# Optimization experiments

Measured on AMD Instinct MI355X. Metric: run time of the kernel, lower is better.

The kernel has to match this reference:

```python
import jax, jax.numpy as jnp
import numpy as np

# Coarse-to-fine lossless 3D segmentation (Seg3dLossless), batch=1, C=1.
RES = [17, 33, 65, 129]          # odd resolutions, stride (RF-1)/(R-1) is integral
RF = RES[-1]
B_MIN, B_MAX = -1.0, 1.0
BAL = 0.5                        # balance_value
N_CONFLICT_ITERS = 2             # fixed unroll of the data-dependent while-loop


def _mlp(pts, w1, b1, w2, b2, w3, b3):
    # query_func: occupancy MLP on normalized (x,y,z) points -> [N]
    h = jax.nn.relu(pts @ w1 + b1)
    h = jax.nn.relu(h @ w2 + b2)
    return jax.nn.sigmoid(h @ w3 + b3)[..., 0]


def _eval_grid(R, w1, b1, w2, b2, w3, b3):
    # batch_eval with align_corners=False: coords2D = (coord + 0.5)/RF, mapped to [B_MIN,B_MAX]
    s = (RF - 1) // (R - 1)
    c = jnp.arange(R, dtype=jnp.float32) * s                 # final-res integer coords
    p = (c + 0.5) / RF * (B_MAX - B_MIN) + B_MIN
    zz, yy, xx = jnp.meshgrid(p, p, p, indexing='ij')        # [D,H,W]
    pts = jnp.stack([xx, yy, zz], axis=-1).reshape(-1, 3)    # (x,y,z) order
    return _mlp(pts, w1, b1, w2, b2, w3, b3).reshape(R, R, R)


def _resize(x, R):
    # trilinear, align_corners=True: out index j -> in coord j*(in-1)/(out-1)
    c = jnp.linspace(0.0, x.shape[0] - 1.0, R)
    zz, yy, xx = jnp.meshgrid(c, c, c, indexing='ij')
    return jax.scipy.ndimage.map_coordinates(x, [zz, yy, xx], order=1, mode='nearest')


def _dilate(m):
    # smooth_conv3x3 (mean filter) followed by >0 == 3x3x3 binary dilation
    f = jax.lax.reduce_window(m.astype(jnp.float32), 0.0, jax.lax.max,
                              (3, 3, 3), (1, 1, 1), 'SAME')
    return f > 0.0


def setup_inputs() -> dict:
    key = jax.random.key(0)
    k1, k2, k3 = jax.random.split(key, 3)
    H = 64
    return {
        'w1': jax.random.normal(k1, (3, H), jnp.float32) * 0.8,
        'b1': jnp.zeros((H,), jnp.float32),
        'w2': jax.random.normal(k2, (H, H), jnp.float32) * (1.0 / np.sqrt(H)),
        'b2': jnp.zeros((H,), jnp.float32),
        'w3': jax.random.normal(k3, (H, 1), jnp.float32) * (1.0 / np.sqrt(H)),
        'b3': jnp.zeros((1,), jnp.float32),
    }


def reference(w1, b1, w2, b2, w3, b3):
    params = (w1, b1, w2, b2, w3, b3)
    # level 0: dense eval on the coarse grid
    occ = _eval_grid(RES[0], *params)                        # [R0,R0,R0]
    s0 = (RF - 1) // (RES[0] - 1)
    calculated = jnp.zeros((RF, RF, RF), bool).at[::s0, ::s0, ::s0].set(True)

    for R in RES[1:]:
        s = (RF - 1) // (R - 1)
        valid = _resize((occ > BAL).astype(jnp.float32), R)  # no-grad mask path
        occ_i = _resize(occ, R)                              # differentiable interp
        boundary = _dilate((valid > 0.0) & (valid < 1.0))
        calc_l = calculated[::s, ::s, ::s]
        boundary = boundary & (~calc_l)                      # skip already-evaluated voxels
        occ_true = _eval_grid(R, *params)                    # query_func at this level
        occ = jnp.where(boundary, occ_true, occ_i)           # scatter of occupancys_topk
        calc_l = calc_l | boundary
        # conflict resolution: re-query 3^3 neighbors of sign-flip voxels
        conflict = boundary & ((occ_i - BAL) * (occ_true - BAL) < 0.0)
        for _ in range(N_CONFLICT_ITERS):
            nbr = _dilate(conflict) & (~calc_l)
            occ_prev = occ
            occ = jnp.where(nbr, occ_true, occ)
            calc_l = calc_l | nbr
            conflict = nbr & ((occ_prev - BAL) * (occ_true - BAL) < 0.0)
        calculated = calculated.at[::s, ::s, ::s].set(calc_l)

    return occ[None, None]                                   # (1, 1, D, H, W)
```

## Files before the change

### kernel.cpp

```cpp
#include <hip/hip_runtime.h>

#define HH 64

static __global__ void k_set_ones(unsigned char* __restrict__ p, int n){
  int i = blockIdx.x * blockDim.x + threadIdx.x;
  if (i < n) p[i] = 1;
}

static __global__ void k_prep_w2t(const float* __restrict__ w2, float* __restrict__ w2t){
  int t = blockIdx.x * 256 + threadIdx.x;
  w2t[t] = w2[(t & 63) * HH + (t >> 6)];
}

__device__ __forceinline__ void mlp_pair(
    const float* __restrict__ sw1,
    const float* __restrict__ sw2t,
    const float* __restrict__ b2, const float* __restrict__ w3,
    const float* __restrict__ b3,
    float xA, float yA, float zA, float xB, float yB, float zB,
    float& outA, float& outB)
{
  const int ibase = ((threadIdx.x & 63) >> 5) * 32;
  float h1a[32], h1b[32];
  #pragma unroll
  for (int k = 0; k < 32; k += 4){
    const float4 wx = *(const float4*)&sw1[      ibase + k];
    const float4 wy = *(const float4*)&sw1[ 64 + ibase + k];
    const float4 wz = *(const float4*)&sw1[128 + ibase + k];
    const float4 bb = *(const float4*)&sw1[192 + ibase + k];
    h1a[k+0] = fmaxf(fmaf(xA,wx.x,fmaf(yA,wy.x,fmaf(zA,wz.x,bb.x))),0.f);
    h1a[k+1] = fmaxf(fmaf(xA,wx.y,fmaf(yA,wy.y,fmaf(zA,wz.y,bb.y))),0.f);
    h1a[k+2] = fmaxf(fmaf(xA,wx.z,fmaf(yA,wy.z,fmaf(zA,wz.z,bb.z))),0.f);
    h1a[k+3] = fmaxf(fmaf(xA,wx.w,fmaf(yA,wy.w,fmaf(zA,wz.w,bb.w))),0.f);
    h1b[k+0] = fmaxf(fmaf(xB,wx.x,fmaf(yB,wy.x,fmaf(zB,wz.x,bb.x))),0.f);
    h1b[k+1] = fmaxf(fmaf(xB,wx.y,fmaf(yB,wy.y,fmaf(zB,wz.y,bb.y))),0.f);
    h1b[k+2] = fmaxf(fmaf(xB,wx.z,fmaf(yB,wy.z,fmaf(zB,wz.z,bb.z))),0.f);
    h1b[k+3] = fmaxf(fmaf(xB,wx.w,fmaf(yB,wy.w,fmaf(zB,wz.w,bb.w))),0.f);
  }
  float oa = b3[0], ob = oa;
  #pragma unroll 1
  for (int j = 0; j < HH; ++j){
    const float4* wrow = (const float4*)&sw2t[j*HH + ibase];
    float a0 = 0.f, a1 = 0.f, c0 = 0.f, c1 = 0.f;
    #pragma unroll
    for (int q = 0; q < 8; q += 2){
      const float4 w0 = wrow[q];
      const float4 w1q = wrow[q+1];
      a0 = fmaf(h1a[4*q+0], w0.x, a0);
      a0 = fmaf(h1a[4*q+1], w0.y, a0);
      a0 = fmaf(h1a[4*q+2], w0.z, a0);
      a0 = fmaf(h1a[4*q+3], w0.w, a0);
      a1 = fmaf(h1a[4*q+4], w1q.x, a1);
      a1 = fmaf(h1a[4*q+5], w1q.y, a1);
      a1 = fmaf(h1a[4*q+6], w1q.z, a1);
      a1 = fmaf(h1a[4*q+7], w1q.w, a1);
      c0 = fmaf(h1b[4*q+0], w0.x, c0);
      c0 = fmaf(h1b[4*q+1], w0.y, c0);
      c0 = fmaf(h1b[4*q+2], w0.z, c0);
      c0 = fmaf(h1b[4*q+3], w0.w, c0);
      c1 = fmaf(h1b[4*q+4], w1q.x, c1);
      c1 = fmaf(h1b[4*q+5], w1q.y, c1);
      c1 = fmaf(h1b[4*q+6], w1q.z, c1);
      c1 = fmaf(h1b[4*q+7], w1q.w, c1);
    }
    float accA = a0 + a1, accB = c0 + c1;
    accA += __shfl_xor(accA, 32);
    accB += __shfl_xor(accB, 32);
    const float bj = b2[j], wj = w3[j];
    oa = fmaf(fmaxf(accA + bj, 0.f), wj, oa);
    ob = fmaf(fmaxf(accB + bj, 0.f), wj, ob);
  }
  outA = 1.f / (1.f + expf(-oa));
  outB = 1.f / (1.f + expf(-ob));
}

#define STAGE_WEIGHTS()                                            \
  __shared__ float sw1[4*HH];                                      \
  __shared__ float sw2t[HH*HH];                                    \
  {                                                                \
    const int t0 = threadIdx.x;                                    \
    if (t0 < 3*HH) sw1[t0] = w1[t0];                               \
    else sw1[t0] = b1[t0 - 3*HH];                                  \
    const float4* s4 = (const float4*)w2t;                         \
    float4* d4 = (float4*)sw2t;                                    \
    for (int i4 = t0; i4 < HH*HH/4; i4 += 256) d4[i4] = s4[i4];    \
    __syncthreads();                                               \
  }

static __global__ __launch_bounds__(256)
__attribute__((amdgpu_waves_per_eu(4,4)))
void k_eval_mlp(
    const float* __restrict__ w1, const float* __restrict__ b1,
    const float* __restrict__ w2t, const float* __restrict__ b2,
    const float* __restrict__ w3, const float* __restrict__ b3,
    float* __restrict__ out, int R, int s)
{
  STAGE_WEIGHTS();
  const unsigned int n = (unsigned int)R * (unsigned int)R * (unsigned int)R;
  const int lane = threadIdx.x & 63;
  const int wid = threadIdx.x >> 6;
  const unsigned int base = blockIdx.x * 256u + (unsigned int)(wid * 64 + (lane & 31));
  const unsigned int pidA = base < n ? base : (n - 1u);
  const unsigned int pB = base + 32u;
  const unsigned int pidB = pB < n ? pB : (n - 1u);
  const float inv129x2 = 2.0f / 129.0f;
  unsigned int cA = pidA % (unsigned int)R, rA = pidA / (unsigned int)R;
  unsigned int cB = pidB % (unsigned int)R, rB = pidB / (unsigned int)R;
  const float xA = ((float)(cA * (unsigned int)s) + 0.5f) * inv129x2 - 1.0f;
  const float yA = ((float)((rA % (unsigned int)R) * (unsigned int)s) + 0.5f) * inv129x2 - 1.0f;
  const float zA = ((float)((rA / (unsigned int)R) * (unsigned int)s) + 0.5f) * inv129x2 - 1.0f;
  const float xB = ((float)(cB * (unsigned int)s) + 0.5f) * inv129x2 - 1.0f;
  const float yB = ((float)((rB % (unsigned int)R) * (unsigned int)s) + 0.5f) * inv129x2 - 1.0f;
  const float zB = ((float)((rB / (unsigned int)R) * (unsigned int)s) + 0.5f) * inv129x2 - 1.0f;
  float oA, oB;
  mlp_pair(sw1, sw2t, b2, w3, b3, xA, yA, zA, xB, yB, zB, oA, oB);
  if ((threadIdx.x & 63) < 32){
    if (base < n) out[pidA] = oA;
    if (pB < n)   out[pidB] = oB;
  }
}

static __global__ __launch_bounds__(256)
__attribute__((amdgpu_waves_per_eu(4,4)))
void k_eval_sparse(
    const float* __restrict__ w1, const float* __restrict__ b1,
    const float* __restrict__ w2t, const float* __restrict__ b2,
    const float* __restrict__ w3, const float* __restrict__ b3,
    const int* __restrict__ idxl, const unsigned int* __restrict__ cnt,
    const float* __restrict__ occ_i,
    float* __restrict__ out, unsigned char* __restrict__ mism,
    int R, int s, unsigned int n)
{
  unsigned int count = *cnt;
  if (count > n) count = n;
  if (blockIdx.x * 256u >= count) return;
  STAGE_WEIGHTS();
  const int lane = threadIdx.x & 63;
  const int wid = threadIdx.x >> 6;
  const unsigned int slotA = blockIdx.x * 256u + (unsigned int)(wid * 64 + (lane & 31));
  const unsigned int slotB = slotA + 32u;
  const bool vA = slotA < count, vB = slotB < count;
  const unsigned int pidA = (unsigned int)idxl[vA ? slotA : 0];
  const unsigned int pidB = (unsigned int)idxl[vB ? slotB : 0];
  const float inv129x2 = 2.0f / 129.0f;
  unsigned int cA = pidA % (unsigned int)R, rA = pidA / (unsigned int)R;
  unsigned int cB = pidB % (unsigned int)R, rB = pidB / (unsigned int)R;
  const float xA = ((float)(cA * (unsigned int)s) + 0.5f) * inv129x2 - 1.0f;
  const float yA = ((float)((rA % (unsigned int)R) * (unsigned int)s) + 0.5f) * inv129x2 - 1.0f;
  const float zA = ((float)((rA / (unsigned int)R) * (unsigned int)s) + 0.5f) * inv129x2 - 1.0f;
  const float xB = ((float)(cB * (unsigned int)s) + 0.5f) * inv129x2 - 1.0f;
  const float yB = ((float)((rB % (unsigned int)R) * (unsigned int)s) + 0.5f) * inv129x2 - 1.0f;
  const float zB = ((float)((rB / (unsigned int)R) * (unsigned int)s) + 0.5f) * inv129x2 - 1.0f;
  float oA, oB;
  mlp_pair(sw1, sw2t, b2, w3, b3, xA, yA, zA, xB, yB, zB, oA, oB);
  if ((threadIdx.x & 63) < 32){
    if (vA){
      out[pidA] = oA;
      mism[pidA] = ((occ_i[pidA] - 0.5f) * (oA - 0.5f) < 0.0f) ? (unsigned char)1 : (unsigned char)0;
    }
    if (vB){
      out[pidB] = oB;
      mism[pidB] = ((occ_i[pidB] - 0.5f) * (oB - 0.5f) < 0.0f) ? (unsigned char)1 : (unsigned char)0;
    }
  }
}

static __global__ __launch_bounds__(256) void k_resize_b0(
    const float* __restrict__ prev,
    const unsigned char* __restrict__ calc_prev,
    float* __restrict__ occ_i, float* __restrict__ occ_out,
    unsigned char* __restrict__ bnd0, unsigned char* __restrict__ calc_out,
    unsigned char* __restrict__ confA, unsigned char* __restrict__ confB,
    unsigned char* __restrict__ upd, int R, int Rp)
{
  const unsigned int n = (unsigned int)R * (unsigned int)R * (unsigned int)R;
  unsigned int gid = blockIdx.x * 256u + threadIdx.x;
  if (gid >= n) return;
  int c = (int)(gid % (unsigned int)R);
  unsigned int r = gid / (unsigned int)R;
  int b = (int)(r % (unsigned int)R);
  int a = (int)(r / (unsigned int)R);
  int a0 = a >> 1, da = a & 1;
  int b0i = b >> 1, db = b & 1;
  int c0 = c >> 1, dc = c & 1;
  float sum = 0.0f;
  int cnt = 0;
  const int tot = (da + 1) * (db + 1) * (dc + 1);
  for (int dz = 0; dz <= da; ++dz)
    for (int dy = 0; dy <= db; ++dy)
      for (int dx = 0; dx <= dc; ++dx){
        float v = prev[((unsigned int)(a0 + dz) * (unsigned int)Rp + (unsigned int)(b0i + dy)) * (unsigned int)Rp + (unsigned int)(c0 + dx)];
        sum += v;
        cnt += (v > 0.5f) ? 1 : 0;
      }
  float oi = sum / (float)tot;
  occ_i[gid] = oi;
  occ_out[gid] = oi;
  bnd0[gid] = (cnt > 0 && cnt < tot) ? 1 : 0;
  calc_out[gid] = ((da | db | dc) == 0)
      ? calc_prev[((unsigned int)a0 * (unsigned int)Rp + (unsigned int)b0i) * (unsigned int)Rp + (unsigned int)c0]
      : (unsigned char)0;
  confA[gid] = 0; confB[gid] = 0; upd[gid] = 0;
}

static __global__ __launch_bounds__(256) void k_resize_boundary(
    const float* __restrict__ prev, const float* __restrict__ occ_true,
    const unsigned char* __restrict__ calc_prev,
    float* __restrict__ occ_i, float* __restrict__ occ_out,
    unsigned char* __restrict__ bnd0,
    unsigned char* __restrict__ mism, unsigned char* __restrict__ calc_out,
    int R, int Rp)
{
  const unsigned int n = (unsigned int)R * (unsigned int)R * (unsigned int)R;
  unsigned int gid = blockIdx.x * 256u + threadIdx.x;
  if (gid >= n) return;
  int c = (int)(gid % (unsigned int)R);
  unsigned int r = gid / (unsigned int)R;
  int b = (int)(r % (unsigned int)R);
  int a = (int)(r / (unsigned int)R);
  int a0 = a >> 1, da = a & 1;
  int b0i = b >> 1, db = b & 1;
  int c0 = c >> 1, dc = c & 1;
  float sum = 0.0f;
  int cnt = 0;
  const int tot = (da + 1) * (db + 1) * (dc + 1);
  for (int dz = 0; dz <= da; ++dz)
    for (int dy = 0; dy <= db; ++dy)
      for (int dx = 0; dx <= dc; ++dx){
        float v = prev[((unsigned int)(a0 + dz) * (unsigned int)Rp + (unsigned int)(b0i + dy)) * (unsigned int)Rp + (unsigned int)(c0 + dx)];
        sum += v;
        cnt += (v > 0.5f) ? 1 : 0;
      }
  float oi = sum / (float)tot;
  occ_i[gid] = oi;
  occ_out[gid] = oi;
  bnd0[gid] = (cnt > 0 && cnt < tot) ? 1 : 0;
  mism[gid] = ((oi - 0.5f) * (occ_true[gid] - 0.5f) < 0.0f) ? 1 : 0;
  calc_out[gid] = ((da | db | dc) == 0)
      ? calc_prev[((unsigned int)a0 * (unsigned int)Rp + (unsigned int)b0i) * (unsigned int)Rp + (unsigned int)c0]
      : (unsigned char)0;
}

static __global__ __launch_bounds__(256) void k_dil7x(
    const unsigned char* __restrict__ in, unsigned char* __restrict__ outp, int R)
{
  const unsigned int n = (unsigned int)R * (unsigned int)R * (unsigned int)R;
  unsigned int gid = blockIdx.x * 256u + threadIdx.x;
  if (gid >= n) return;
  int c = (int)(gid % (unsigned int)R);
  int g = (int)gid;
  int m = 0;
  #pragma unroll
  for (int d = -3; d <= 3; ++d){
    int q = c + d;
    if (q >= 0 && q < R) m |= in[g + d];
  }
  outp[gid] = (unsigned char)(m ? 1 : 0);
}

static __global__ __launch_bounds__(256) void k_dil7y(
    const unsigned char* __restrict__ in, unsigned char* __restrict__ outp, int R)
{
  const unsigned int n = (unsigned int)R * (unsigned int)R * (unsigned int)R;
  unsigned int gid = blockIdx.x * 256u + threadIdx.x;
  if (gid >= n) return;
  unsigned int r = gid / (unsigned int)R;
  int b = (int)(r % (unsigned int)R);
  int g = (int)gid;
  int m = 0;
  #pragma unroll
  for (int d = -3; d <= 3; ++d){
    int q = b + d;
    if (q >= 0 && q < R) m |= in[g + d * R];
  }
  outp[gid] = (unsigned char)(m ? 1 : 0);
}

static __global__ __launch_bounds__(256) void k_dil7z_count(
    const unsigned char* __restrict__ in, unsigned char* __restrict__ outp,
    unsigned int* __restrict__ bcnt, int R)
{
  const unsigned int n = (unsigned int)R * (unsigned int)R * (unsigned int)R;
  unsigned int gid = blockIdx.x * 256u + threadIdx.x;
  int m = 0;
  if (gid < n){
    int a = (int)(gid / ((unsigned int)R * (unsigned int)R));
    int g = (int)gid;
    int RR = R * R;
    #pragma unroll
    for (int d = -3; d <= 3; ++d){
      int q = a + d;
      if (q >= 0 && q < R) m |= in[g + d * RR];
    }
    outp[gid] = (unsigned char)(m ? 1 : 0);
  }
  unsigned long long bm = __ballot(m != 0);
  __shared__ unsigned int wc[4];
  int wid = (int)(threadIdx.x >> 6);
  if ((threadIdx.x & 63u) == 0) wc[wid] = (unsigned int)__popcll(bm);
  __syncthreads();
  if (threadIdx.x == 0) bcnt[blockIdx.x] = wc[0] + wc[1] + wc[2] + wc[3];
}

static __global__ __launch_bounds__(1024) void k_scan(
    unsigned int* __restrict__ bcnt, unsigned int nb, unsigned int* __restrict__ total)
{
  __shared__ unsigned int part[1024];
  const unsigned int t = threadIdx.x;
  const unsigned int chunk = (nb + 1023u) / 1024u;
  const unsigned int beg = t * chunk;
  const unsigned int end = (beg + chunk < nb) ? (beg + chunk) : nb;
  unsigned int s = 0;
  for (unsigned int i = beg; i < end; ++i) s += bcnt[i];
  part[t] = s;
  __syncthreads();
  for (int offd = 1; offd < 1024; offd <<= 1){
    unsigned int v = (t >= (unsigned int)offd) ? part[t - offd] : 0u;
    __syncthreads();
    part[t] += v;
    __syncthreads();
  }
  unsigned int run = (t == 0) ? 0u : part[t - 1];
  for (unsigned int i = beg; i < end; ++i){
    unsigned int v = bcnt[i];
    bcnt[i] = run;
    run += v;
  }
  if (t == 1023) *total = part[1023];
}

static __global__ __launch_bounds__(256) void k_scatter(
    const unsigned char* __restrict__ cand, const unsigned int* __restrict__ boff,
    int* __restrict__ idxl, unsigned int n)
{
  unsigned int gid = blockIdx.x * 256u + threadIdx.x;
  bool pred = (gid < n) && (cand[gid] != 0);
  unsigned long long m = __ballot(pred);
  __shared__ unsigned int wbase[4];
  int wid = (int)(threadIdx.x >> 6);
  int lane = (int)(threadIdx.x & 63u);
  if (lane == 0) wbase[wid] = (unsigned int)__popcll(m);
  __syncthreads();
  if (threadIdx.x == 0){
    unsigned int b = boff[blockIdx.x];
    unsigned int t0 = wbase[0], t1 = wbase[1], t2 = wbase[2];
    wbase[0] = b; wbase[1] = b + t0; wbase[2] = b + t0 + t1; wbase[3] = b + t0 + t1 + t2;
  }
  __syncthreads();
  if (pred){
    int pre = __popcll(m & ((1ull << lane) - 1ull));
    idxl[wbase[wid] + (unsigned int)pre] = (int)gid;
  }
}

static __global__ __launch_bounds__(256) void k_dilate_sparse(
    const int* __restrict__ idxl, const unsigned int* __restrict__ cnt,
    const unsigned char* __restrict__ src, const unsigned char* __restrict__ mism,
    unsigned char* __restrict__ calc, unsigned char* __restrict__ conf_out,
    unsigned char* __restrict__ upd, int R, int final_step,
    const float* __restrict__ occ_true, float* __restrict__ occ_out,
    unsigned int n)
{
  unsigned int count = *cnt;
  if (count > n) count = n;
  for (unsigned int slot = blockIdx.x * 256u + threadIdx.x; slot < count;
       slot += gridDim.x * 256u){
    int gid = idxl[slot];
    int c = gid % R;
    int r = gid / R;
    int b = r % R;
    int a = r / R;
    int m = 0;
    for (int dz = -1; dz <= 1; ++dz){
      int az = a + dz; if (az < 0 || az >= R) continue;
      for (int dy = -1; dy <= 1; ++dy){
        int by = b + dy; if (by < 0 || by >= R) continue;
        for (int dx = -1; dx <= 1; ++dx){
          int cx = c + dx; if (cx < 0 || cx >= R) continue;
          m |= src[(az * R + by) * R + cx];
        }
      }
    }
    unsigned char nb = (m && !calc[gid]) ? (unsigned char)1 : (unsigned char)0;
    conf_out[gid] = (nb && mism[gid]) ? (unsigned char)1 : (unsigned char)0;
    unsigned char u = upd[gid];
    if (nb){ calc[gid] = 1; if (!u){ upd[gid] = 1; u = 1; } }
    if (final_step && u) occ_out[gid] = occ_true[gid];
  }
}

static __global__ __launch_bounds__(256) void k_dilate_step(
    const unsigned char* __restrict__ src, const unsigned char* __restrict__ mism,
    unsigned char* __restrict__ calc, unsigned char* __restrict__ conf_out,
    unsigned char* __restrict__ upd, int R, int first, int final_step,
    const float* __restrict__ occ_true, float* __restrict__ occ_out)
{
  const unsigned int n = (unsigned int)R * (unsigned int)R * (unsigned int)R;
  unsigned int gid = blockIdx.x * 256u + threadIdx.x;
  if (gid >= n) return;
  int c = (int)(gid % (unsigned int)R);
  unsigned int r = gid / (unsigned int)R;
  int b = (int)(r % (unsigned int)R);
  int a = (int)(r / (unsigned int)R);
  int m = 0;
  for (int dz = -1; dz <= 1; ++dz){
    int az = a + dz; if (az < 0 || az >= R) continue;
    for (int dy = -1; dy <= 1; ++dy){
      int by = b + dy; if (by < 0 || by >= R) continue;
      for (int dx = -1; dx <= 1; ++dx){
        int cx = c + dx; if (cx < 0 || cx >= R) continue;
        m |= src[((unsigned int)az * (unsigned int)R + (unsigned int)by) * (unsigned int)R + (unsigned int)cx];
      }
    }
  }
  unsigned char nb = (m && !calc[gid]) ? (unsigned char)1 : (unsigned char)0;
  if (nb) calc[gid] = 1;
  conf_out[gid] = (nb && mism[gid]) ? (unsigned char)1 : (unsigned char)0;
  unsigned char u;
  if (first){ u = nb; upd[gid] = nb; }
  else { u = upd[gid]; if (nb && !u){ upd[gid] = 1; u = 1; } }
  if (final_step && u) occ_out[gid] = occ_true[gid];
}

extern "C" void kernel_launch(void* const* d_in, const int* in_sizes, int n_in,
                              void* d_out, int out_size, void* d_ws, size_t ws_size,
                              hipStream_t stream)
{
  const float* w1 = (const float*)d_in[0];
  const float* b1 = (const float*)d_in[1];
  const float* w2 = (const float*)d_in[2];
  const float* b2 = (const float*)d_in[3];
  const float* w3 = (const float*)d_in[4];
  const float* b3 = (const float*)d_in[5];
  float* out = (float*)d_out;

  const int NF = 129 * 129 * 129;
  const int NP = 65 * 65 * 65;
  char* ws = (char*)d_ws;
  size_t off = 0;
  auto alloc = [&](size_t bytes) -> void* {
    void* p = (void*)(ws + off);
    off += (bytes + 255) & ~(size_t)255;
    return p;
  };
  float* f_true  = (float*)alloc((size_t)NF * 4);
  float* f_occi  = (float*)alloc((size_t)NF * 4);
  float* f_prevA = (float*)alloc((size_t)NP * 4);
  float* f_prevB = (float*)alloc((size_t)NP * 4);
  float* f_w2t   = (float*)alloc((size_t)HH * HH * 4);
  int*   i_idx   = (int*)alloc((size_t)NF * 4);
  unsigned int* u_cnt  = (unsigned int*)alloc(256);
  unsigned int* u_bcnt = (unsigned int*)alloc(8448 * 4);
  unsigned char* b_b0    = (unsigned char*)alloc(NF);
  unsigned char* b_mism  = (unsigned char*)alloc(NF);
  unsigned char* b_confA = (unsigned char*)alloc(NF);
  unsigned char* b_confB = (unsigned char*)alloc(NF);
  unsigned char* b_calcA = (unsigned char*)alloc(NF);
  unsigned char* b_calcB = (unsigned char*)alloc(NF);
  unsigned char* b_upd   = (unsigned char*)alloc(NF);
  unsigned char* b_cand  = (unsigned char*)alloc(NF);
  unsigned char* b_tmp   = (unsigned char*)alloc(NF);
  (void)ws_size;

  k_prep_w2t<<<16, 256, 0, stream>>>(w2, f_w2t);

  {
    int R = 17, s = 8;
    int n = R * R * R;
    int blocks = (n + 255) / 256;
    k_eval_mlp<<<blocks, 256, 0, stream>>>(w1, b1, f_w2t, b2, w3, b3, f_prevA, R, s);
    k_set_ones<<<blocks, 256, 0, stream>>>(b_calcA, n);
  }

  int Rp = 17;
  float* prev = f_prevA;
  unsigned char* calcP = b_calcA;
  unsigned char* calcC = b_calcB;
  for (int li = 1; li <= 3; ++li){
    int R = 2 * Rp - 1;
    int s = 128 / (R - 1);
    unsigned int n = (unsigned int)R * (unsigned int)R * (unsigned int)R;
    int blocks = (int)((n + 255u) / 256u);
    float* occ_out = (li == 3) ? out : ((prev == f_prevA) ? f_prevB : f_prevA);

    if (R == 33){
      k_eval_mlp<<<blocks, 256, 0, stream>>>(w1, b1, f_w2t, b2, w3, b3, f_true, R, s);
      k_resize_boundary<<<blocks, 256, 0, stream>>>(prev, f_true, calcP, f_occi, occ_out, b_b0, b_mism, calcC, R, Rp);
      k_dilate_step<<<blocks, 256, 0, stream>>>(b_b0,    b_mism, calcC, b_confA, b_upd, R, 1, 0, f_true, occ_out);
      k_dilate_step<<<blocks, 256, 0, stream>>>(b_confA, b_mism, calcC, b_confB, b_upd, R, 0, 0, f_true, occ_out);
      k_dilate_step<<<blocks, 256, 0, stream>>>(b_confB, b_mism, calcC, b_confA, b_upd, R, 0, 1, f_true, occ_out);
    } else {
      k_resize_b0<<<blocks, 256, 0, stream>>>(prev, calcP, f_occi, occ_out, b_b0, calcC,
                                              b_confA, b_confB, b_upd, R, Rp);
      k_dil7x<<<blocks, 256, 0, stream>>>(b_b0,  b_tmp,  R);
      k_dil7y<<<blocks, 256, 0, stream>>>(b_tmp, b_cand, R);
      k_dil7z_count<<<blocks, 256, 0, stream>>>(b_cand, b_tmp, u_bcnt, R);
      k_scan<<<1, 1024, 0, stream>>>(u_bcnt, (unsigned int)blocks, u_cnt);
      k_scatter<<<blocks, 256, 0, stream>>>(b_tmp, u_bcnt, i_idx, n);
      k_eval_sparse<<<blocks, 256, 0, stream>>>(
          w1, b1, f_w2t, b2, w3, b3, i_idx, u_cnt, f_occi, f_true, b_mism, R, s, n);
      int sblocks = blocks < 4096 ? blocks : 4096;
      k_dilate_sparse<<<sblocks, 256, 0, stream>>>(i_idx, u_cnt, b_b0,    b_mism, calcC, b_confA, b_upd, R, 0, f_true, occ_out, n);
      k_dilate_sparse<<<sblocks, 256, 0, stream>>>(i_idx, u_cnt, b_confA, b_mism, calcC, b_confB, b_upd, R, 0, f_true, occ_out, n);
      k_dilate_sparse<<<sblocks, 256, 0, stream>>>(i_idx, u_cnt, b_confB, b_mism, calcC, b_confA, b_upd, R, 1, f_true, occ_out, n);
    }

    prev = occ_out;
    unsigned char* tmpc = calcP; calcP = calcC; calcC = tmpc;
    Rp = R;
  }
  (void)in_sizes; (void)n_in; (void)out_size;
}
```

Before: 307.4 us.

## Evaluate MLP one point per thread reading weights directly from global memory

Replaces the paired-point, split-hidden-dimension MLP (two points per thread, halves reduced with a cross-lane shuffle, weights staged in LDS) with a one-point-per-thread version. Each thread keeps all 64 hidden activations in registers and reads w1/w2t/b2/w3 straight from global memory through uniform loads, so the shared-memory staging and its __syncthreads are gone. This raises per-thread register pressure (64-float array under a 4-waves-per-EU bound) and depends on the weight loads being wave-uniform and cached, which could cause spills or slower weight fetches.

New measurement: 348.3 us. 13.3% more time.

```diff
diff --git a/kernel.cpp b/kernel.cpp
--- a/kernel.cpp
+++ b/kernel.cpp
@@ -12,80 +12,32 @@
   w2t[t] = w2[(t & 63) * HH + (t >> 6)];
 }
 
-__device__ __forceinline__ void mlp_pair(
-    const float* __restrict__ sw1,
-    const float* __restrict__ sw2t,
-    const float* __restrict__ b2, const float* __restrict__ w3,
-    const float* __restrict__ b3,
-    float xA, float yA, float zA, float xB, float yB, float zB,
-    float& outA, float& outB)
-{
-  const int ibase = ((threadIdx.x & 63) >> 5) * 32;
-  float h1a[32], h1b[32];
+__device__ __forceinline__ float mlp_point(
+    const float* __restrict__ w1, const float* __restrict__ b1,
+    const float* __restrict__ w2t, const float* __restrict__ b2,
+    const float* __restrict__ w3, const float* __restrict__ b3,
+    float x, float y, float z)
+{
+  float h[HH];
   #pragma unroll
-  for (int k = 0; k < 32; k += 4){
-    const float4 wx = *(const float4*)&sw1[      ibase + k];
-    const float4 wy = *(const float4*)&sw1[ 64 + ibase + k];
-    const float4 wz = *(const float4*)&sw1[128 + ibase + k];
-    const float4 bb = *(const float4*)&sw1[192 + ibase + k];
-    h1a[k+0] = fmaxf(fmaf(xA,wx.x,fmaf(yA,wy.x,fmaf(zA,wz.x,bb.x))),0.f);
-    h1a[k+1] = fmaxf(fmaf(xA,wx.y,fmaf(yA,wy.y,fmaf(zA,wz.y,bb.y))),0.f);
-    h1a[k+2] = fmaxf(fmaf(xA,wx.z,fmaf(yA,wy.z,fmaf(zA,wz.z,bb.z))),0.f);
-    h1a[k+3] = fmaxf(fmaf(xA,wx.w,fmaf(yA,wy.w,fmaf(zA,wz.w,bb.w))),0.f);
-    h1b[k+0] = fmaxf(fmaf(xB,wx.x,fmaf(yB,wy.x,fmaf(zB,wz.x,bb.x))),0.f);
-    h1b[k+1] = fmaxf(fmaf(xB,wx.y,fmaf(yB,wy.y,fmaf(zB,wz.y,bb.y))),0.f);
-    h1b[k+2] = fmaxf(fmaf(xB,wx.z,fmaf(yB,wy.z,fmaf(zB,wz.z,bb.z))),0.f);
-    h1b[k+3] = fmaxf(fmaf(xB,wx.w,fmaf(yB,wy.w,fmaf(zB,wz.w,bb.w))),0.f);
-  }
-  float oa = b3[0], ob = oa;
-  #pragma unroll 1
+  for (int k = 0; k < HH; ++k)
+    h[k] = fmaxf(fmaf(x, w1[k], fmaf(y, w1[HH + k], fmaf(z, w1[2*HH + k], b1[k]))), 0.f);
+  float o = b3[0];
+  #pragma unroll 2
   for (int j = 0; j < HH; ++j){
-    const float4* wrow = (const float4*)&sw2t[j*HH + ibase];
-    float a0 = 0.f, a1 = 0.f, c0 = 0.f, c1 = 0.f;
+    const float* __restrict__ row = w2t + j * HH;
+    float a0 = 0.f, a1 = 0.f, a2 = 0.f, a3 = 0.f;
     #pragma unroll
-    for (int q = 0; q < 8; q += 2){
-      const float4 w0 = wrow[q];
-      const float4 w1q = wrow[q+1];
-      a0 = fmaf(h1a[4*q+0], w0.x, a0);
-      a0 = fmaf(h1a[4*q+1], w0.y, a0);
-      a0 = fmaf(h1a[4*q+2], w0.z, a0);
-      a0 = fmaf(h1a[4*q+3], w0.w, a0);
-      a1 = fmaf(h1a[4*q+4], w1q.x, a1);
-      a1 = fmaf(h1a[4*q+5], w1q.y, a1);
-      a1 = fmaf(h1a[4*q+6], w1q.z, a1);
-      a1 = fmaf(h1a[4*q+7], w1q.w, a1);
-      c0 = fmaf(h1b[4*q+0], w0.x, c0);
-      c0 = fmaf(h1b[4*q+1], w0.y, c0);
-      c0 = fmaf(h1b[4*q+2], w0.z, c0);
-      c0 = fmaf(h1b[4*q+3], w0.w, c0);
-      c1 = fmaf(h1b[4*q+4], w1q.x, c1);
-      c1 = fmaf(h1b[4*q+5], w1q.y, c1);
-      c1 = fmaf(h1b[4*q+6], w1q.z, c1);
-      c1 = fmaf(h1b[4*q+7], w1q.w, c1);
+    for (int k = 0; k < 16; ++k){
+      a0 = fmaf(h[k     ], row[k     ], a0);
+      a1 = fmaf(h[k + 16], row[k + 16], a1);
+      a2 = fmaf(h[k + 32], row[k + 32], a2);
+      a3 = fmaf(h[k + 48], row[k + 48], a3);
     }
-    float accA = a0 + a1, accB = c0 + c1;
-    accA += __shfl_xor(accA, 32);
-    accB += __shfl_xor(accB, 32);
-    const float bj = b2[j], wj = w3[j];
-    oa = fmaf(fmaxf(accA + bj, 0.f), wj, oa);
-    ob = fmaf(fmaxf(accB + bj, 0.f), wj, ob);
-  }
-  outA = 1.f / (1.f + expf(-oa));
-  outB = 1.f / (1.f + expf(-ob));
-}
-
-#define STAGE_WEIGHTS()                                            \
-  __shared__ float sw1[4*HH];                                      \
-  __shared__ float sw2t[HH*HH];                                    \
-  {                                                                \
-    const int t0 = threadIdx.x;                                    \
-    if (t0 < 3*HH) sw1[t0] = w1[t0];                               \
-    else sw1[t0] = b1[t0 - 3*HH];                                  \
-    const float4* s4 = (const float4*)w2t;                         \
-    float4* d4 = (float4*)sw2t;                                    \
-    for (int i4 = t0; i4 < HH*HH/4; i4 += 256) d4[i4] = s4[i4];    \
-    __syncthreads();                                               \
-  }
+    o = fmaf(fmaxf((a0 + a1) + (a2 + a3) + b2[j], 0.f), w3[j], o);
+  }
+  return 1.f / (1.f + expf(-o));
+}
 
 static __global__ __launch_bounds__(256)
 __attribute__((amdgpu_waves_per_eu(4,4)))
@@ -95,29 +47,16 @@
     const float* __restrict__ w3, const float* __restrict__ b3,
     float* __restrict__ out, int R, int s)
 {
-  STAGE_WEIGHTS();
-  const unsigned int n = (unsigned int)R * (unsigned int)R * (unsigned int)R;
-  const int lane = threadIdx.x & 63;
-  const int wid = threadIdx.x >> 6;
-  const unsigned int base = blockIdx.x * 256u + (unsigned int)(wid * 64 + (lane & 31));
-  const unsigned int pidA = base < n ? base : (n - 1u);
-  const unsigned int pB = base + 32u;
-  const unsigned int pidB = pB < n ? pB : (n - 1u);
+  const unsigned int n = (unsigned int)R * (unsigned int)R * (unsigned int)R;
+  const unsigned int gid = blockIdx.x * 256u + threadIdx.x;
+  const unsigned int pid = gid < n ? gid : (n - 1u);
   const float inv129x2 = 2.0f / 129.0f;
-  unsigned int cA = pidA % (unsigned int)R, rA = pidA / (unsigned int)R;
-  unsigned int cB = pidB % (unsigned int)R, rB = pidB / (unsigned int)R;
-  const float xA = ((float)(cA * (unsigned int)s) + 0.5f) * inv129x2 - 1.0f;
-  const float yA = ((float)((rA % (unsigned int)R) * (unsigned int)s) + 0.5f) * inv129x2 - 1.0f;
-  const float zA = ((float)((rA / (unsigned int)R) * (unsigned int)s) + 0.5f) * inv129x2 - 1.0f;
-  const float xB = ((float)(cB * (unsigned int)s) + 0.5f) * inv129x2 - 1.0f;
-  const float yB = ((float)((rB % (unsigned int)R) * (unsigned int)s) + 0.5f) * inv129x2 - 1.0f;
-  const float zB = ((float)((rB / (unsigned int)R) * (unsigned int)s) + 0.5f) * inv129x2 - 1.0f;
-  float oA, oB;
-  mlp_pair(sw1, sw2t, b2, w3, b3, xA, yA, zA, xB, yB, zB, oA, oB);
-  if ((threadIdx.x & 63) < 32){
-    if (base < n) out[pidA] = oA;
-    if (pB < n)   out[pidB] = oB;
-  }
+  unsigned int c = pid % (unsigned int)R, r = pid / (unsigned int)R;
+  const float x = ((float)(c * (unsigned int)s) + 0.5f) * inv129x2 - 1.0f;
+  const float y = ((float)((r % (unsigned int)R) * (unsigned int)s) + 0.5f) * inv129x2 - 1.0f;
+  const float z = ((float)((r / (unsigned int)R) * (unsigned int)s) + 0.5f) * inv129x2 - 1.0f;
+  float o = mlp_point(w1, b1, w2t, b2, w3, b3, x, y, z);
+  if (gid < n) out[pid] = o;
 }
 
 static __global__ __launch_bounds__(256)
@@ -134,34 +73,18 @@
   unsigned int count = *cnt;
   if (count > n) count = n;
   if (blockIdx.x * 256u >= count) return;
-  STAGE_WEIGHTS();
-  const int lane = threadIdx.x & 63;
-  const int wid = threadIdx.x >> 6;
-  const unsigned int slotA = blockIdx.x * 256u + (unsigned int)(wid * 64 + (lane & 31));
-  const unsigned int slotB = slotA + 32u;
-  const bool vA = slotA < count, vB = slotB < count;
-  const unsigned int pidA = (unsigned int)idxl[vA ? slotA : 0];
-  const unsigned int pidB = (unsigned int)idxl[vB ? slotB : 0];
+  const unsigned int slot = blockIdx.x * 256u + threadIdx.x;
+  const bool v = slot < count;
+  const unsigned int pid = (unsigned int)idxl[v ? slot : 0];
   const float inv129x2 = 2.0f / 129.0f;
-  unsigned int cA = pidA % (unsigned int)R, rA = pidA / (unsigned int)R;
-  unsigned int cB = pidB % (unsigned int)R, rB = pidB / (unsigned int)R;
-  const float xA = ((float)(cA * (unsigned int)s) + 0.5f) * inv129x2 - 1.0f;
-  const float yA = ((float)((rA % (unsigned int)R) * (unsigned int)s) + 0.5f) * inv129x2 - 1.0f;
-  const float zA = ((float)((rA / (unsigned int)R) * (unsigned int)s) + 0.5f) * inv129x2 - 1.0f;
-  const float xB = ((float)(cB * (unsigned int)s) + 0.5f) * inv129x2 - 1.0f;
-  const float yB = ((float)((rB % (unsigned int)R) * (unsigned int)s) + 0.5f) * inv129x2 - 1.0f;
-  const float zB = ((float)((rB / (unsigned int)R) * (unsigned int)s) + 0.5f) * inv129x2 - 1.0f;
-  float oA, oB;
-  mlp_pair(sw1, sw2t, b2, w3, b3, xA, yA, zA, xB, yB, zB, oA, oB);
-  if ((threadIdx.x & 63) < 32){
-    if (vA){
-      out[pidA] = oA;
-      mism[pidA] = ((occ_i[pidA] - 0.5f) * (oA - 0.5f) < 0.0f) ? (unsigned char)1 : (unsigned char)0;
-    }
-    if (vB){
-      out[pidB] = oB;
-      mism[pidB] = ((occ_i[pidB] - 0.5f) * (oB - 0.5f) < 0.0f) ? (unsigned char)1 : (unsigned char)0;
-    }
+  unsigned int c = pid % (unsigned int)R, r = pid / (unsigned int)R;
+  const float x = ((float)(c * (unsigned int)s) + 0.5f) * inv129x2 - 1.0f;
+  const float y = ((float)((r % (unsigned int)R) * (unsigned int)s) + 0.5f) * inv129x2 - 1.0f;
+  const float z = ((float)((r / (unsigned int)R) * (unsigned int)s) + 0.5f) * inv129x2 - 1.0f;
+  float o = mlp_point(w1, b1, w2t, b2, w3, b3, x, y, z);
+  if (v){
+    out[pid] = o;
+    mism[pid] = ((occ_i[pid] - 0.5f) * (o - 0.5f) < 0.0f) ? (unsigned char)1 : (unsigned char)0;
   }
 }
 
```

## Read packed W2 rows with bias and w3 from global instead of LDS staging

Applied to the files above, without the earlier changes.

Stops staging the 64x64 transposed W2 matrix into shared memory in every block of the MLP kernels. The kernels now read weights straight from a global buffer whose rows are padded to 72 floats, with b2[j] and w3[j] stored next to each row so one float2 load fetches both. This removes the per-block 16KB LDS copy and its barrier and cuts LDS use, which could raise occupancy. In exchange every inner-loop weight load becomes a global/L1-cached load (uniform across half-waves) instead of an LDS read, which may have higher latency.

Result: slower. 366.0 us (+19.0%).

```diff
diff --git a/kernel.cpp b/kernel.cpp
--- a/kernel.cpp
+++ b/kernel.cpp
@@ -1,21 +1,30 @@
 #include <hip/hip_runtime.h>
 
 #define HH 64
+#define RSTRIDE 72
 
 static __global__ void k_set_ones(unsigned char* __restrict__ p, int n){
   int i = blockIdx.x * blockDim.x + threadIdx.x;
   if (i < n) p[i] = 1;
 }
 
-static __global__ void k_prep_w2t(const float* __restrict__ w2, float* __restrict__ w2t){
+static __global__ void k_prep_pack(const float* __restrict__ w2,
+                                   const float* __restrict__ b2,
+                                   const float* __restrict__ w3,
+                                   float* __restrict__ w2tp){
   int t = blockIdx.x * 256 + threadIdx.x;
-  w2t[t] = w2[(t & 63) * HH + (t >> 6)];
+  if (t >= HH * RSTRIDE) return;
+  int row = t / RSTRIDE, c = t - row * RSTRIDE;
+  float v = 0.f;
+  if (c < HH) v = w2[c * HH + row];
+  else if (c == HH) v = b2[row];
+  else if (c == HH + 1) v = w3[row];
+  w2tp[t] = v;
 }
 
 __device__ __forceinline__ void mlp_pair(
     const float* __restrict__ sw1,
-    const float* __restrict__ sw2t,
-    const float* __restrict__ b2, const float* __restrict__ w3,
+    const float* __restrict__ w2tp,
     const float* __restrict__ b3,
     float xA, float yA, float zA, float xB, float yB, float zB,
     float& outA, float& outB)
@@ -40,7 +49,8 @@
   float oa = b3[0], ob = oa;
   #pragma unroll 1
   for (int j = 0; j < HH; ++j){
-    const float4* wrow = (const float4*)&sw2t[j*HH + ibase];
+    const float* __restrict__ rowp = w2tp + j * RSTRIDE;
+    const float4* __restrict__ wrow = (const float4*)(rowp + ibase);
     float a0 = 0.f, a1 = 0.f, c0 = 0.f, c1 = 0.f;
     #pragma unroll
     for (int q = 0; q < 8; q += 2){
@@ -66,24 +76,20 @@
     float accA = a0 + a1, accB = c0 + c1;
     accA += __shfl_xor(accA, 32);
     accB += __shfl_xor(accB, 32);
-    const float bj = b2[j], wj = w3[j];
-    oa = fmaf(fmaxf(accA + bj, 0.f), wj, oa);
-    ob = fmaf(fmaxf(accB + bj, 0.f), wj, ob);
+    const float2 bw = *(const float2*)(rowp + HH);
+    oa = fmaf(fmaxf(accA + bw.x, 0.f), bw.y, oa);
+    ob = fmaf(fmaxf(accB + bw.x, 0.f), bw.y, ob);
   }
   outA = 1.f / (1.f + expf(-oa));
   outB = 1.f / (1.f + expf(-ob));
 }
 
-#define STAGE_WEIGHTS()                                            \
+#define STAGE_W1()                                                 \
   __shared__ float sw1[4*HH];                                      \
-  __shared__ float sw2t[HH*HH];                                    \
   {                                                                \
     const int t0 = threadIdx.x;                                    \
     if (t0 < 3*HH) sw1[t0] = w1[t0];                               \
-    else sw1[t0] = b1[t0 - 3*HH];                                  \
-    const float4* s4 = (const float4*)w2t;                         \
-    float4* d4 = (float4*)sw2t;                                    \
-    for (int i4 = t0; i4 < HH*HH/4; i4 += 256) d4[i4] = s4[i4];    \
+    else if (t0 < 4*HH) sw1[t0] = b1[t0 - 3*HH];                   \
     __syncthreads();                                               \
   }
 
@@ -91,11 +97,10 @@
 __attribute__((amdgpu_waves_per_eu(4,4)))
 void k_eval_mlp(
     const float* __restrict__ w1, const float* __restrict__ b1,
-    const float* __restrict__ w2t, const float* __restrict__ b2,
-    const float* __restrict__ w3, const float* __restrict__ b3,
+    const float* __restrict__ w2tp, const float* __restrict__ b3,
     float* __restrict__ out, int R, int s)
 {
-  STAGE_WEIGHTS();
+  STAGE_W1();
   const unsigned int n = (unsigned int)R * (unsigned int)R * (unsigned int)R;
   const int lane = threadIdx.x & 63;
   const int wid = threadIdx.x >> 6;
@@ -113,7 +118,7 @@
   const float yB = ((float)((rB % (unsigned int)R) * (unsigned int)s) + 0.5f) * inv129x2 - 1.0f;
   const float zB = ((float)((rB / (unsigned int)R) * (unsigned int)s) + 0.5f) * inv129x2 - 1.0f;
   float oA, oB;
-  mlp_pair(sw1, sw2t, b2, w3, b3, xA, yA, zA, xB, yB, zB, oA, oB);
+  mlp_pair(sw1, w2tp, b3, xA, yA, zA, xB, yB, zB, oA, oB);
   if ((threadIdx.x & 63) < 32){
     if (base < n) out[pidA] = oA;
     if (pB < n)   out[pidB] = oB;
@@ -124,8 +129,7 @@
 __attribute__((amdgpu_waves_per_eu(4,4)))
 void k_eval_sparse(
     const float* __restrict__ w1, const float* __restrict__ b1,
-    const float* __restrict__ w2t, const float* __restrict__ b2,
-    const float* __restrict__ w3, const float* __restrict__ b3,
+    const float* __restrict__ w2tp, const float* __restrict__ b3,
     const int* __restrict__ idxl, const unsigned int* __restrict__ cnt,
     const float* __restrict__ occ_i,
     float* __restrict__ out, unsigned char* __restrict__ mism,
@@ -134,7 +138,7 @@
   unsigned int count = *cnt;
   if (count > n) count = n;
   if (blockIdx.x * 256u >= count) return;
-  STAGE_WEIGHTS();
+  STAGE_W1();
   const int lane = threadIdx.x & 63;
   const int wid = threadIdx.x >> 6;
   const unsigned int slotA = blockIdx.x * 256u + (unsigned int)(wid * 64 + (lane & 31));
@@ -152,7 +156,7 @@
   const float yB = ((float)((rB % (unsigned int)R) * (unsigned int)s) + 0.5f) * inv129x2 - 1.0f;
   const float zB = ((float)((rB / (unsigned int)R) * (unsigned int)s) + 0.5f) * inv129x2 - 1.0f;
   float oA, oB;
-  mlp_pair(sw1, sw2t, b2, w3, b3, xA, yA, zA, xB, yB, zB, oA, oB);
+  mlp_pair(sw1, w2tp, b3, xA, yA, zA, xB, yB, zB, oA, oB);
   if ((threadIdx.x & 63) < 32){
     if (vA){
       out[pidA] = oA;
@@ -447,7 +451,7 @@
   float* f_occi  = (float*)alloc((size_t)NF * 4);
   float* f_prevA = (float*)alloc((size_t)NP * 4);
   float* f_prevB = (float*)alloc((size_t)NP * 4);
-  float* f_w2t   = (float*)alloc((size_t)HH * HH * 4);
+  float* f_w2tp  = (float*)alloc((size_t)HH * RSTRIDE * 4);
   int*   i_idx   = (int*)alloc((size_t)NF * 4);
   unsigned int* u_cnt  = (unsigned int*)alloc(256);
   unsigned int* u_bcnt = (unsigned int*)alloc(8448 * 4);
@@ -462,13 +466,13 @@
   unsigned char* b_tmp   = (unsigned char*)alloc(NF);
   (void)ws_size;
 
-  k_prep_w2t<<<16, 256, 0, stream>>>(w2, f_w2t);
+  k_prep_pack<<<(HH * RSTRIDE + 255) / 256, 256, 0, stream>>>(w2, b2, w3, f_w2tp);
 
   {
     int R = 17, s = 8;
     int n = R * R * R;
     int blocks = (n + 255) / 256;
-    k_eval_mlp<<<blocks, 256, 0, stream>>>(w1, b1, f_w2t, b2, w3, b3, f_prevA, R, s);
+    k_eval_mlp<<<blocks, 256, 0, stream>>>(w1, b1, f_w2tp, b3, f_prevA, R, s);
     k_set_ones<<<blocks, 256, 0, stream>>>(b_calcA, n);
   }
 
@@ -484,7 +488,7 @@
     float* occ_out = (li == 3) ? out : ((prev == f_prevA) ? f_prevB : f_prevA);
 
     if (R == 33){
-      k_eval_mlp<<<blocks, 256, 0, stream>>>(w1, b1, f_w2t, b2, w3, b3, f_true, R, s);
+      k_eval_mlp<<<blocks, 256, 0, stream>>>(w1, b1, f_w2tp, b3, f_true, R, s);
       k_resize_boundary<<<blocks, 256, 0, stream>>>(prev, f_true, calcP, f_occi, occ_out, b_b0, b_mism, calcC, R, Rp);
       k_dilate_step<<<blocks, 256, 0, stream>>>(b_b0,    b_mism, calcC, b_confA, b_upd, R, 1, 0, f_true, occ_out);
       k_dilate_step<<<blocks, 256, 0, stream>>>(b_confA, b_mism, calcC, b_confB, b_upd, R, 0, 0, f_true, occ_out);
@@ -498,7 +502,7 @@
       k_scan<<<1, 1024, 0, stream>>>(u_bcnt, (unsigned int)blocks, u_cnt);
       k_scatter<<<blocks, 256, 0, stream>>>(b_tmp, u_bcnt, i_idx, n);
       k_eval_sparse<<<blocks, 256, 0, stream>>>(
-          w1, b1, f_w2t, b2, w3, b3, i_idx, u_cnt, f_occi, f_true, b_mism, R, s, n);
+          w1, b1, f_w2tp, b3, i_idx, u_cnt, f_occi, f_true, b_mism, R, s, n);
       int sblocks = blocks < 4096 ? blocks : 4096;
       k_dilate_sparse<<<sblocks, 256, 0, stream>>>(i_idx, u_cnt, b_b0,    b_mism, calcC, b_confA, b_upd, R, 0, f_true, occ_out, n);
       k_dilate_sparse<<<sblocks, 256, 0, stream>>>(i_idx, u_cnt, b_confA, b_mism, calcC, b_confB, b_upd, R, 0, f_true, occ_out, n);
```
